# Performance work log

Measured on AMD Instinct MI355X. Metric: run time of the kernel, lower is better.

The kernel has to match this reference:

```python
import jax, jax.numpy as jnp
import numpy as np

IGNORE = 255
THRESH = 0.7
MIN_KEPT = 100000
AUX_W = 1.0


def resize_bilinear_ac(x, oh, ow):
    # F.interpolate(..., mode='bilinear', align_corners=True); x: (b,c,h,w)
    b, c, h, w = x.shape
    ys = jnp.linspace(0.0, h - 1.0, oh)
    xs = jnp.linspace(0.0, w - 1.0, ow)
    y0 = jnp.floor(ys).astype(jnp.int32)
    x0 = jnp.floor(xs).astype(jnp.int32)
    y1 = jnp.minimum(y0 + 1, h - 1)
    x1 = jnp.minimum(x0 + 1, w - 1)
    wy = (ys - y0)[:, None]          # (oh,1) broadcasts over (b,c,oh,w)
    wx = xs - x0                     # (ow,)
    rows = x[:, :, y0, :] * (1.0 - wy) + x[:, :, y1, :] * wy   # (b,c,oh,w)
    return rows[:, :, :, x0] * (1.0 - wx) + rows[:, :, :, x1] * wx


def ohem_ce(pred, target):
    # pred: (b,c,h,w) logits, target: (b,h,w) int labels
    b, c, h, w = pred.shape
    n = b * h * w
    t = target.reshape(-1)
    valid = t != IGNORE
    t_cl = jnp.where(valid, t, 0)
    logits = pred.transpose(0, 2, 3, 1).reshape(n, c)
    logp = jax.nn.log_softmax(logits, axis=-1)
    pix = jnp.arange(n)
    logp_t = logp[pix, t_cl]
    # prob at target class; invalid pixels filled with 1 (as in masked_fill_)
    mask_prob = jnp.where(valid, jnp.exp(logp_t), 1.0)
    idx = min(n, MIN_KEPT) - 1
    thr = jnp.maximum(jnp.asarray(THRESH, pred.dtype), jnp.sort(mask_prob)[idx])
    kept = mask_prob <= thr
    final_valid = valid & kept
    nll = -logp_t
    denom = jnp.maximum(final_valid.sum(), 1).astype(pred.dtype)
    return jnp.sum(jnp.where(final_valid, nll, 0.0)) / denom


def boundary_bce(p, t):
    # p: (n,1,h,w) probs, t: (n,1,h,w) binary targets; per-sample pos/neg weights
    pos = jnp.sum(t == 1.0, axis=(1, 2, 3), keepdims=True).astype(p.dtype)
    neg = jnp.sum(t == 0.0, axis=(1, 2, 3), keepdims=True).astype(p.dtype)
    valid = pos + neg
    wgt = jnp.where(t == 1.0, neg / valid, jnp.where(t == 0.0, pos / valid, 0.0))
    logp = jnp.clip(jnp.log(p), -100.0)          # torch BCELoss clamps log at -100
    log1mp = jnp.clip(jnp.log(1.0 - p), -100.0)
    bce = -(t * logp + (1.0 - t) * log1mp)
    return jnp.mean(wgt * bce)


def setup_inputs() -> dict:
    key = jax.random.key(0)
    k1, k2, k3, k4, k5 = jax.random.split(key, 5)
    main_pred = jax.random.normal(k1, (4, 19, 64, 128), dtype=jnp.float32)
    coarse_pred = jax.random.normal(k2, (4, 19, 64, 128), dtype=jnp.float32)
    boundary_pred = jax.random.uniform(k3, (4, 1, 64, 128), dtype=jnp.float32)
    seg_gt = jax.random.randint(k4, (4, 512, 1024), 0, 19, dtype=jnp.int32)
    boundary_gt = jax.random.randint(k5, (4, 1, 512, 1024), 0, 2).astype(jnp.float32)
    return {"main_pred": main_pred, "coarse_pred": coarse_pred,
            "boundary_pred": boundary_pred, "seg_gt": seg_gt,
            "boundary_gt": boundary_gt}


def reference(main_pred, coarse_pred, boundary_pred, seg_gt, boundary_gt):
    h, w = seg_gt.shape[1], seg_gt.shape[2]
    main_up = resize_bilinear_ac(main_pred, h, w)
    loss = ohem_ce(main_up, seg_gt)
    coarse_up = resize_bilinear_ac(coarse_pred, h, w)
    loss = loss + AUX_W * ohem_ce(coarse_up, seg_gt)
    bound_up = resize_bilinear_ac(boundary_pred, h, w)
    loss = loss + boundary_bce(bound_up, boundary_gt)
    return loss
```

## Files before the change

### kernel.cpp

```cpp
#include <hip/hip_runtime.h>

#define NPX    2097152
#define NPX4   (NPX/4)
#define CH_STR 8192
#define IMG_STR 155648

#define OFF_CTL   (2ull*NPX*4)
#define CTL_HIST    0
#define CTL_BAR     24576
#define CTL_PREFIX  24578
#define CTL_KREM    24580
#define CTL_THR     24582
#define CTL_PPSUM   24584
#define CTL_PPCNT   28680
#define CTL_OPSUM   32776
#define CTL_OPCNT   33288
#define CTL_BPS     33800
#define CTL_BPC     34824

__global__ __launch_bounds__(256) void fused_pass1(
    const float* __restrict__ mp, const float* __restrict__ cp,
    const float* __restrict__ bp, const int* __restrict__ seg,
    const float* __restrict__ bg,
    float* __restrict__ probA, float* __restrict__ ppsum, unsigned* __restrict__ ppcnt,
    float* __restrict__ bps, unsigned* __restrict__ bpc, unsigned* __restrict__ bar)
{
    __shared__ float2 erow[19 * 128];
    __shared__ float rf[4]; __shared__ unsigned ru[4];
    __shared__ float rf2[4]; __shared__ unsigned ru2[4];
    int bk = blockIdx.x;
    int tid = threadIdx.x;

    if (bk == 0 && tid < 2) bar[tid] = 0u;

    if (bk < 4096) {
        int head = bk >> 11;
        int task = bk & 2047;
        int b = task >> 9;
        int y = task & 511;
        const float* pred = head ? cp : mp;

        float fy = (float)y * (63.0f / 511.0f);
        int y0 = min((int)fy, 63);
        int y1 = min(y0 + 1, 63);
        float wy = fy - (float)y0;

        const float* r0 = pred + (size_t)b * IMG_STR + y0 * 128;
        const float* r1 = pred + (size_t)b * IMG_STR + y1 * 128;
        for (int i = tid; i < 2432; i += 256) {
            int c = i >> 7, x = i & 127;
            float v0 = r0[c * CH_STR + x];
            float v1 = r1[c * CH_STR + x];
            float e = fmaf(wy, v1 - v0, v0);
            erow[c * 128 + x].x = e;
            if (x > 0)    erow[c * 128 + x - 1].y = e;
            if (x == 127) erow[c * 128 + 127].y = e;
        }
        __syncthreads();

        int xb = tid << 2;
        int P = (b * 512 + y) * 1024 + xb;
        int4 t4 = *(const int4*)(seg + P);
        int t[4] = {t4.x, t4.y, t4.z, t4.w};

        float fx0 = (float)xb * (127.0f / 1023.0f);
        int X = min((int)fx0, 126);
        float wA[4], wB[4], wC[4];
#pragma unroll
        for (int dx = 0; dx < 4; ++dx) {
            float fx = (float)(xb + dx) * (127.0f / 1023.0f);
            int x0 = min((int)fx, 127);
            float wx = fx - (float)x0;
            bool sm = (x0 == X);
            wA[dx] = sm ? (1.0f - wx) : 0.0f;
            wB[dx] = sm ? wx : (1.0f - wx);
            wC[dx] = sm ? 0.0f : wx;
        }

        float s[4] = {0.f, 0.f, 0.f, 0.f};
        for (int c = 0; c < 19; ++c) {
            float2 eA = erow[c * 128 + X];
            float2 eB = erow[c * 128 + X + 1];
#pragma unroll
            for (int dx = 0; dx < 4; ++dx) {
                float l = fmaf(eA.x, wA[dx], fmaf(eA.y, wB[dx], eB.y * wC[dx]));
                s[dx] += __expf(l);
            }
        }

        float fs = 0.f; unsigned ic = 0;
        float pr[4];
#pragma unroll
        for (int dx = 0; dx < 4; ++dx) {
            bool valid = (t[dx] != 255);
            int tc = valid ? t[dx] : 0;
            float2 eA = erow[tc * 128 + X];
            float2 eB = erow[tc * 128 + X + 1];
            float lt = fmaf(eA.x, wA[dx], fmaf(eA.y, wB[dx], eB.y * wC[dx]));
            float ls = __logf(s[dx]);
            float n  = ls - lt;
            float p  = fminf(__expf(-n), 1.0f);
            pr[dx] = valid ? p : 1.0f;
            if (valid && p <= 0.7f) { fs += n; ic++; }
        }
        *(float4*)(probA + (size_t)head * NPX + P) = make_float4(pr[0], pr[1], pr[2], pr[3]);

        for (int o = 32; o; o >>= 1) {
            fs += __shfl_down(fs, o, 64);
            ic += (unsigned)__shfl_down((int)ic, o, 64);
        }
        int wave = tid >> 6, lane = tid & 63;
        if (lane == 0) { rf[wave] = fs; ru[wave] = ic; }
        __syncthreads();
        if (tid == 0) {
            ppsum[head * 2048 + task] = rf[0] + rf[1] + rf[2] + rf[3];
            ppcnt[head * 2048 + task] = ru[0] + ru[1] + ru[2] + ru[3];
        }
    } else {
        int bb = bk - 4096;
        int b  = bb >> 7;
        int blk = bb & 127;
        float psum = 0.f, nsum = 0.f; unsigned pc = 0, nc = 0;

        for (int g = blk * 256 + tid; g < 131072; g += 128 * 256) {
            int P = g << 2;
            int y = P >> 10, xb = P & 1023;

            float fy = (float)y * (63.0f / 511.0f);
            int y0 = min((int)fy, 63);
            int y1 = min(y0 + 1, 63);
            float wy = fy - (float)y0;

            const float* r0 = bp + b * 8192 + y0 * 128;
            const float* r1 = bp + b * 8192 + y1 * 128;
            float fx0 = (float)xb * (127.0f / 1023.0f);
            int X  = min((int)fx0, 126);
            int X2 = min(X + 2, 127);
            float c0 = r0[X], c1 = r0[X + 1], c2 = r0[X2];
            float d0 = r1[X], d1 = r1[X + 1], d2 = r1[X2];
            float e0 = fmaf(wy, d0 - c0, c0);
            float e1 = fmaf(wy, d1 - c1, c1);
            float e2 = fmaf(wy, d2 - c2, c2);

            float4 t4 = *(const float4*)(bg + (size_t)b * 524288 + P);
            float tv[4] = {t4.x, t4.y, t4.z, t4.w};

#pragma unroll
            for (int dx = 0; dx < 4; ++dx) {
                float fx = (float)(xb + dx) * (127.0f / 1023.0f);
                int x0 = min((int)fx, 127);
                int x1 = min(x0 + 1, 127);
                float wx = fx - (float)x0;
                float a0 = (x0 == X)     ? e0 : e1;
                float a1 = (x1 == X + 1) ? e1 : e2;
                float p  = fmaf(wx, a1 - a0, a0);
                bool isp = (tv[dx] == 1.0f);
                bool isn = (tv[dx] == 0.0f);
                float q = isp ? p : 1.0f - p;
                float l = fmaxf(__logf(q), -100.0f);
                if (isp) { pc++; psum -= l; }
                if (isn) { nc++; nsum -= l; }
            }
        }
        for (int o = 32; o; o >>= 1) {
            psum += __shfl_down(psum, o, 64);
            nsum += __shfl_down(nsum, o, 64);
            pc   += (unsigned)__shfl_down((int)pc, o, 64);
            nc   += (unsigned)__shfl_down((int)nc, o, 64);
        }
        int wave = tid >> 6, lane = tid & 63;
        if (lane == 0) { rf[wave] = psum; rf2[wave] = nsum; ru[wave] = pc; ru2[wave] = nc; }
        __syncthreads();
        if (tid == 0) {
            bps[2 * bb]     = rf[0] + rf[1] + rf[2] + rf[3];
            bps[2 * bb + 1] = rf2[0] + rf2[1] + rf2[2] + rf2[3];
            bpc[2 * bb]     = ru[0] + ru[1] + ru[2] + ru[3];
            bpc[2 * bb + 1] = ru2[0] + ru2[1] + ru2[2] + ru2[3];
        }
    }
}

__device__ __forceinline__ void gbar(unsigned* bar, int tid) {
    __syncthreads();
    if (tid == 0) {
        unsigned g = __hip_atomic_load(&bar[1], __ATOMIC_RELAXED, __HIP_MEMORY_SCOPE_AGENT);
        unsigned t = __hip_atomic_fetch_add(&bar[0], 1u, __ATOMIC_ACQ_REL, __HIP_MEMORY_SCOPE_AGENT);
        if (t == 255u) {
            __hip_atomic_store(&bar[0], 0u, __ATOMIC_RELAXED, __HIP_MEMORY_SCOPE_AGENT);
            __hip_atomic_store(&bar[1], g + 1u, __ATOMIC_RELEASE, __HIP_MEMORY_SCOPE_AGENT);
        } else {
            while (__hip_atomic_load(&bar[1], __ATOMIC_ACQUIRE, __HIP_MEMORY_SCOPE_AGENT) == g)
                __builtin_amdgcn_s_sleep(8);
        }
    }
    __syncthreads();
}

__device__ void combine_out(int tid, float headLossSum,
                            const float* __restrict__ bps, const unsigned* __restrict__ bpc,
                            float* __restrict__ out)
{
    __shared__ float lf[256]; __shared__ unsigned lu[256];
    __shared__ float Pb[4], Nb[4]; __shared__ unsigned PCb[4], NCb[4];
    for (int b = 0; b < 4; ++b) {
        float ps = 0.f, ns = 0.f; unsigned p_c = 0, n_c = 0;
        if (tid < 128) {
            int j = b * 128 + tid;
            ps = bps[2 * j]; ns = bps[2 * j + 1];
            p_c = bpc[2 * j]; n_c = bpc[2 * j + 1];
        }
        lf[tid] = ps; lu[tid] = p_c; __syncthreads();
        for (int o = 128; o; o >>= 1) {
            if (tid < o) { lf[tid] += lf[tid + o]; lu[tid] += lu[tid + o]; }
            __syncthreads();
        }
        if (tid == 0) { Pb[b] = lf[0]; PCb[b] = lu[0]; }
        __syncthreads();
        lf[tid] = ns; lu[tid] = n_c; __syncthreads();
        for (int o = 128; o; o >>= 1) {
            if (tid < o) { lf[tid] += lf[tid + o]; lu[tid] += lu[tid + o]; }
            __syncthreads();
        }
        if (tid == 0) { Nb[b] = lf[0]; NCb[b] = lu[0]; }
        __syncthreads();
    }
    if (tid == 0) {
        float bt = 0.f;
        for (int b = 0; b < 4; ++b) {
            float pos = (float)PCb[b], neg = (float)NCb[b];
            float val = fmaxf(pos + neg, 1.f);
            bt += (neg / val) * Pb[b] + (pos / val) * Nb[b];
        }
        out[0] = headLossSum + bt / 2097152.0f;
    }
}

__global__ __launch_bounds__(256) void finish_all(
    const float* __restrict__ probA, const int* __restrict__ seg,
    const float* __restrict__ ppsum, const unsigned* __restrict__ ppcnt,
    const float* __restrict__ bps, const unsigned* __restrict__ bpc,
    unsigned* __restrict__ hist, unsigned* __restrict__ bar,
    unsigned* __restrict__ prefix, unsigned* __restrict__ krem,
    float* __restrict__ thr,
    float* __restrict__ opsum, unsigned* __restrict__ opcnt,
    float* __restrict__ out)
{
    int tid = threadIdx.x, blk = blockIdx.x;
    int wave = tid >> 6, lane = tid & 63;

    float s0 = 0.f, s1 = 0.f; unsigned c0 = 0u, c1 = 0u;
    for (int i = tid; i < 2048; i += 256) {
        s0 += ppsum[i];        c0 += ppcnt[i];
        s1 += ppsum[2048 + i]; c1 += ppcnt[2048 + i];
    }
    for (int o = 32; o; o >>= 1) {
        s0 += __shfl_down(s0, o, 64); s1 += __shfl_down(s1, o, 64);
        c0 += (unsigned)__shfl_down((int)c0, o, 64);
        c1 += (unsigned)__shfl_down((int)c1, o, 64);
    }
    __shared__ float ws0[4], ws1[4]; __shared__ unsigned wc0[4], wc1[4];
    if (lane == 0) { ws0[wave] = s0; ws1[wave] = s1; wc0[wave] = c0; wc1[wave] = c1; }
    __syncthreads();
    float S0 = ws0[0] + ws0[1] + ws0[2] + ws0[3];
    float S1 = ws1[0] + ws1[1] + ws1[2] + ws1[3];
    unsigned C0 = wc0[0] + wc0[1] + wc0[2] + wc0[3];
    unsigned C1 = wc1[0] + wc1[1] + wc1[2] + wc1[3];
    bool done0 = C0 >= 100000u, done1 = C1 >= 100000u;

    if (done0 && done1) {
        if (blk == 0)
            combine_out(tid, S0 / fmaxf((float)C0, 1.f) + S1 / fmaxf((float)C1, 1.f),
                        bps, bpc, out);
        return;
    }

    __shared__ unsigned hsh[4096];
    __shared__ unsigned cpre[257];
    unsigned doneMask = (done0 ? 1u : 0u) | (done1 ? 2u : 0u);

    for (int i = blk * 256 + tid; i < 24576; i += 65536) hist[i] = 0u;
    gbar(bar, tid);

    for (int lvl = 0; lvl < 3; ++lvl) {
        unsigned* hl = hist + lvl * 8192;
        for (int h = 0; h < 2; ++h) {
            if (doneMask & (1u << h)) continue;
            unsigned pre = (lvl == 0) ? 0u : prefix[h];
            for (int i = tid; i < 4096; i += 256) hsh[i] = 0u;
            __syncthreads();
            const float4* prob = (const float4*)(probA + (size_t)h * NPX);
            for (int i = blk * 256 + tid; i < NPX4; i += 65536) {
                float4 p = prob[i];
                unsigned u[4] = {__float_as_uint(p.x), __float_as_uint(p.y),
                                 __float_as_uint(p.z), __float_as_uint(p.w)};
#pragma unroll
                for (int k = 0; k < 4; ++k) {
                    unsigned bv = u[k];
                    if (lvl == 0)      atomicAdd(&hsh[bv >> 18], 1u);
                    else if (lvl == 1) { if ((bv >> 18) == pre) atomicAdd(&hsh[(bv >> 6) & 0xFFFu], 1u); }
                    else               { if ((bv >> 6) == pre) atomicAdd(&hsh[bv & 63u], 1u); }
                }
            }
            __syncthreads();
            for (int i = tid; i < 4096; i += 256) {
                unsigned v = hsh[i];
                if (v) atomicAdd(&hl[h * 4096 + i], v);
            }
            __syncthreads();
        }
        gbar(bar, tid);
        if (blk == 0) {
            int bins = (lvl == 2) ? 64 : 4096;
            for (int h = 0; h < 2; ++h) {
                if (doneMask & (1u << h)) continue;
                const unsigned* hh = hl + h * 4096;
                int per = (bins + 255) >> 8;
                int base = tid * per;
                unsigned ssum = 0;
                for (int i = 0; i < per; ++i) { int idx = base + i; if (idx < bins) ssum += hh[idx]; }
                cpre[tid] = ssum; __syncthreads();
                if (tid == 0) {
                    unsigned acc = 0;
                    for (int i = 0; i < 256; ++i) { unsigned v = cpre[i]; cpre[i] = acc; acc += v; }
                    cpre[256] = acc;
                }
                __syncthreads();
                unsigned K = (lvl == 0) ? 100000u : krem[h];
                unsigned my = cpre[tid], nx = cpre[tid + 1];
                if (K > 0 && my < K && K <= nx) {
                    unsigned acc = my;
                    for (int i = 0; i < per; ++i) {
                        int idx = base + i;
                        unsigned c = (idx < bins) ? hh[idx] : 0u;
                        if (acc < K && K <= acc + c) {
                            if (lvl == 0)      { prefix[h] = (unsigned)idx; krem[h] = K - acc; }
                            else if (lvl == 1) { prefix[h] = (prefix[h] << 12) | (unsigned)idx; krem[h] = K - acc; }
                            else {
                                unsigned bitsv = (prefix[h] << 6) | (unsigned)idx;
                                thr[h] = fmaxf(0.7f, __uint_as_float(bitsv));
                            }
                            break;
                        }
                        acc += c;
                    }
                }
                __syncthreads();
            }
        }
        gbar(bar, tid);
    }

    for (int h = 0; h < 2; ++h) {
        if (doneMask & (1u << h)) continue;
        float th = thr[h];
        const float4* prob = (const float4*)(probA + (size_t)h * NPX);
        const int4*   sg4  = (const int4*)seg;
        float fs = 0.f; unsigned ic = 0;
        for (int i = blk * 256 + tid; i < NPX4; i += 65536) {
            float4 p = prob[i]; int4 tt = sg4[i];
            if (tt.x != 255 && p.x <= th) { fs -= __logf(p.x); ic++; }
            if (tt.y != 255 && p.y <= th) { fs -= __logf(p.y); ic++; }
            if (tt.z != 255 && p.z <= th) { fs -= __logf(p.z); ic++; }
            if (tt.w != 255 && p.w <= th) { fs -= __logf(p.w); ic++; }
        }
        for (int o = 32; o; o >>= 1) {
            fs += __shfl_down(fs, o, 64);
            ic += (unsigned)__shfl_down((int)ic, o, 64);
        }
        __shared__ float wf[4]; __shared__ unsigned wu[4];
        if (lane == 0) { wf[wave] = fs; wu[wave] = ic; }
        __syncthreads();
        if (tid == 0) {
            opsum[h * 256 + blk] = wf[0] + wf[1] + wf[2] + wf[3];
            opcnt[h * 256 + blk] = wu[0] + wu[1] + wu[2] + wu[3];
        }
        __syncthreads();
    }
    gbar(bar, tid);
    if (blk == 0) {
        __shared__ float lf2[256]; __shared__ unsigned lu2[256];
        float hls = 0.f;
        for (int h = 0; h < 2; ++h) {
            float S; unsigned C;
            if (doneMask & (1u << h)) {
                S = h ? S1 : S0; C = h ? C1 : C0;
            } else {
                lf2[tid] = opsum[h * 256 + tid]; lu2[tid] = opcnt[h * 256 + tid];
                __syncthreads();
                for (int o = 128; o; o >>= 1) {
                    if (tid < o) { lf2[tid] += lf2[tid + o]; lu2[tid] += lu2[tid + o]; }
                    __syncthreads();
                }
                S = lf2[0]; C = lu2[0];
                __syncthreads();
            }
            hls += S / fmaxf((float)C, 1.f);
        }
        combine_out(tid, hls, bps, bpc, out);
    }
}

extern "C" void kernel_launch(void* const* d_in, const int* in_sizes, int n_in,
                              void* d_out, int out_size, void* d_ws, size_t ws_size,
                              hipStream_t stream)
{
    const float* mp  = (const float*)d_in[0];
    const float* cp  = (const float*)d_in[1];
    const float* bp  = (const float*)d_in[2];
    const int*   seg = (const int*)d_in[3];
    const float* bg  = (const float*)d_in[4];
    float* out = (float*)d_out;

    char* ws = (char*)d_ws;
    float* probA = (float*)ws;
    unsigned* ctl    = (unsigned*)(ws + OFF_CTL);
    unsigned* hist   = ctl + CTL_HIST;
    unsigned* bar    = ctl + CTL_BAR;
    unsigned* prefix = ctl + CTL_PREFIX;
    unsigned* krem   = ctl + CTL_KREM;
    float*    thr    = (float*)(ctl + CTL_THR);
    float*    ppsum  = (float*)(ctl + CTL_PPSUM);
    unsigned* ppcnt  = ctl + CTL_PPCNT;
    float*    opsum  = (float*)(ctl + CTL_OPSUM);
    unsigned* opcnt  = ctl + CTL_OPCNT;
    float*    bps    = (float*)(ctl + CTL_BPS);
    unsigned* bpc    = ctl + CTL_BPC;

    fused_pass1<<<dim3(4608), 256, 0, stream>>>(mp, cp, bp, seg, bg, probA,
                                                ppsum, ppcnt, bps, bpc, bar);
    finish_all<<<dim3(256), 256, 0, stream>>>(probA, seg, ppsum, ppcnt, bps, bpc,
                                              hist, bar, prefix, krem, thr,
                                              opsum, opcnt, out);
}
```

Measured before the change: 110.1 us.

## Skip OHEM threshold selection when enough pixels fall below the threshold

The last block to finish the first pass, found with an atomic counter, reduces the per-block loss sums and counts. If both heads have at least MIN_KEPT pixels whose target probability is at or below THRESH, the sorted k-th value cannot exceed THRESH, so the threshold is exactly THRESH. In that case this block writes the final loss directly and sets a flag that makes finish_all return at once, skipping the histogram and radix-select passes and their grid barriers. The cost is one atomic per block plus a serial tail in one block. There is also a possible race: block 0 resets the counter while other blocks may already be incrementing it.

After: 321.8 us. 2.92x slower.

```diff
diff --git a/kernel.cpp b/kernel.cpp
--- a/kernel.cpp
+++ b/kernel.cpp
@@ -17,21 +17,33 @@
 #define CTL_OPCNT   33288
 #define CTL_BPS     33800
 #define CTL_BPC     34824
+#define CTL_CNT     35848
+#define CTL_FLAG    35849
+
+#define MAGIC_FAST 0x3A9C67E5u
+#define MAGIC_SLOW 0x3A9C67E6u
+#define GRID_P1    4608u
 
 __global__ __launch_bounds__(256) void fused_pass1(
     const float* __restrict__ mp, const float* __restrict__ cp,
     const float* __restrict__ bp, const int* __restrict__ seg,
     const float* __restrict__ bg,
     float* __restrict__ probA, float* __restrict__ ppsum, unsigned* __restrict__ ppcnt,
-    float* __restrict__ bps, unsigned* __restrict__ bpc, unsigned* __restrict__ bar)
+    float* __restrict__ bps, unsigned* __restrict__ bpc, unsigned* __restrict__ bar,
+    unsigned* __restrict__ cnt, unsigned* __restrict__ flag,
+    float* __restrict__ out)
 {
     __shared__ float2 erow[19 * 128];
     __shared__ float rf[4]; __shared__ unsigned ru[4];
     __shared__ float rf2[4]; __shared__ unsigned ru2[4];
+    __shared__ unsigned amLast;
+    __shared__ float Pb[4], Nb[4]; __shared__ unsigned PCb[4], NCb[4];
     int bk = blockIdx.x;
     int tid = threadIdx.x;
 
     if (bk == 0 && tid < 2) bar[tid] = 0u;
+    if (bk == 0 && tid == 0)
+        __hip_atomic_store(cnt, 0u, __ATOMIC_RELAXED, __HIP_MEMORY_SCOPE_AGENT);
 
     if (bk < 4096) {
         int head = bk >> 11;
@@ -178,6 +190,79 @@
             bpc[2 * bb + 1] = ru2[0] + ru2[1] + ru2[2] + ru2[3];
         }
     }
+
+    __syncthreads();
+    if (tid == 0) {
+        __threadfence();
+        unsigned old = __hip_atomic_fetch_add(cnt, 1u, __ATOMIC_ACQ_REL,
+                                              __HIP_MEMORY_SCOPE_AGENT);
+        amLast = (old == GRID_P1 - 1u) ? 1u : 0u;
+    }
+    __syncthreads();
+    if (!amLast) return;
+    __threadfence();
+
+    float s0 = 0.f, s1 = 0.f; unsigned c0 = 0u, c1 = 0u;
+    for (int i = tid; i < 2048; i += 256) {
+        s0 += ppsum[i];        c0 += ppcnt[i];
+        s1 += ppsum[2048 + i]; c1 += ppcnt[2048 + i];
+    }
+    for (int o = 32; o; o >>= 1) {
+        s0 += __shfl_down(s0, o, 64); s1 += __shfl_down(s1, o, 64);
+        c0 += (unsigned)__shfl_down((int)c0, o, 64);
+        c1 += (unsigned)__shfl_down((int)c1, o, 64);
+    }
+    int wv = tid >> 6, ln = tid & 63;
+    if (ln == 0) { rf[wv] = s0; rf2[wv] = s1; ru[wv] = c0; ru2[wv] = c1; }
+    __syncthreads();
+    float S0 = rf[0] + rf[1] + rf[2] + rf[3];
+    float S1 = rf2[0] + rf2[1] + rf2[2] + rf2[3];
+    unsigned C0 = ru[0] + ru[1] + ru[2] + ru[3];
+    unsigned C1 = ru2[0] + ru2[1] + ru2[2] + ru2[3];
+    bool fast = (C0 >= 100000u) && (C1 >= 100000u);
+
+    if (fast) {
+        float*    lf = (float*)erow;
+        unsigned* lu = (unsigned*)erow + 256;
+        for (int b = 0; b < 4; ++b) {
+            float ps = 0.f, ns = 0.f; unsigned p_c = 0, n_c = 0;
+            if (tid < 128) {
+                int j = b * 128 + tid;
+                ps = bps[2 * j]; ns = bps[2 * j + 1];
+                p_c = bpc[2 * j]; n_c = bpc[2 * j + 1];
+            }
+            lf[tid] = ps; lu[tid] = p_c; __syncthreads();
+            for (int o = 128; o; o >>= 1) {
+                if (tid < o) { lf[tid] += lf[tid + o]; lu[tid] += lu[tid + o]; }
+                __syncthreads();
+            }
+            if (tid == 0) { Pb[b] = lf[0]; PCb[b] = lu[0]; }
+            __syncthreads();
+            lf[tid] = ns; lu[tid] = n_c; __syncthreads();
+            for (int o = 128; o; o >>= 1) {
+                if (tid < o) { lf[tid] += lf[tid + o]; lu[tid] += lu[tid + o]; }
+                __syncthreads();
+            }
+            if (tid == 0) { Nb[b] = lf[0]; NCb[b] = lu[0]; }
+            __syncthreads();
+        }
+        if (tid == 0) {
+            float bt = 0.f;
+            for (int b = 0; b < 4; ++b) {
+                float pos = (float)PCb[b], neg = (float)NCb[b];
+                float val = fmaxf(pos + neg, 1.f);
+                bt += (neg / val) * Pb[b] + (pos / val) * Nb[b];
+            }
+            float hls = S0 / fmaxf((float)C0, 1.f) + S1 / fmaxf((float)C1, 1.f);
+            out[0] = hls + bt / 2097152.0f;
+        }
+    }
+    __syncthreads();
+    if (tid == 0) {
+        __threadfence();
+        __hip_atomic_store(flag, fast ? MAGIC_FAST : MAGIC_SLOW,
+                           __ATOMIC_RELEASE, __HIP_MEMORY_SCOPE_AGENT);
+    }
 }
 
 __device__ __forceinline__ void gbar(unsigned* bar, int tid) {
@@ -243,8 +328,12 @@
     unsigned* __restrict__ prefix, unsigned* __restrict__ krem,
     float* __restrict__ thr,
     float* __restrict__ opsum, unsigned* __restrict__ opcnt,
+    unsigned* __restrict__ flag,
     float* __restrict__ out)
 {
+    if (__hip_atomic_load(flag, __ATOMIC_ACQUIRE, __HIP_MEMORY_SCOPE_AGENT) == MAGIC_FAST)
+        return;
+
     int tid = threadIdx.x, blk = blockIdx.x;
     int wave = tid >> 6, lane = tid & 63;
 
@@ -425,10 +514,13 @@
     unsigned* opcnt  = ctl + CTL_OPCNT;
     float*    bps    = (float*)(ctl + CTL_BPS);
     unsigned* bpc    = ctl + CTL_BPC;
-
-    fused_pass1<<<dim3(4608), 256, 0, stream>>>(mp, cp, bp, seg, bg, probA,
-                                                ppsum, ppcnt, bps, bpc, bar);
+    unsigned* cnt    = ctl + CTL_CNT;
+    unsigned* flag   = ctl + CTL_FLAG;
+
+    fused_pass1<<<dim3(GRID_P1), 256, 0, stream>>>(mp, cp, bp, seg, bg, probA,
+                                                   ppsum, ppcnt, bps, bpc, bar,
+                                                   cnt, flag, out);
     finish_all<<<dim3(256), 256, 0, stream>>>(probA, seg, ppsum, ppcnt, bps, bpc,
                                               hist, bar, prefix, krem, thr,
-                                              opsum, opcnt, out);
+                                              opsum, opcnt, flag, out);
 }
```
